# Optimization experiments

Measured on AMD Instinct MI355X. Metric: run time of the kernel, lower is better.

## Reference

```python
import jax, jax.numpy as jnp
import numpy as np

N, E, H, NH = 50000, 800000, 128, 4
D = H // NH
EPS = 1e-5


def _ln(x, g, b):
    m = jnp.mean(x, axis=-1, keepdims=True)
    v = jnp.mean((x - m) ** 2, axis=-1, keepdims=True)
    return (x - m) * jax.lax.rsqrt(v + EPS) * g + b


def setup_inputs() -> dict:
    key = jax.random.key(0)
    ks = jax.random.split(key, 16)

    def lin(k, fi, fo):
        w = jax.random.normal(k, (fi, fo), jnp.float32) * (1.0 / np.sqrt(fi))
        return w, jnp.zeros((fo,), jnp.float32)

    h = jax.random.normal(ks[0], (N, H), jnp.float32)
    e = jax.random.normal(ks[1], (E, H), jnp.float32)
    src = jax.random.randint(ks[2], (E,), 0, N, jnp.int32)
    dst = jax.random.randint(ks[3], (E,), 0, N, jnp.int32)

    Wq, bq = lin(ks[4], H, H)
    Wk, bk = lin(ks[5], 2 * H, H)
    Wv, bv = lin(ks[6], 2 * H, H)
    Wn1, bn1 = lin(ks[7], H, H)
    Wn2, bn2 = lin(ks[8], H, H)
    We1, be1 = lin(ks[9], 3 * H, H)
    We2, be2 = lin(ks[10], H, H)
    gh = jnp.ones((H,), jnp.float32)
    bh = jnp.zeros((H,), jnp.float32)
    ge = jnp.ones((H,), jnp.float32)
    be = jnp.zeros((H,), jnp.float32)

    return dict(h=h, e=e, src=src, dst=dst, Wq=Wq, bq=bq, Wk=Wk, bk=bk,
                Wv=Wv, bv=bv, Wn1=Wn1, bn1=bn1, Wn2=Wn2, bn2=bn2,
                We1=We1, be1=be1, We2=We2, be2=be2, gh=gh, bh=bh, ge=ge, be=be)


def reference(h, e, src, dst, Wq, bq, Wk, bk, Wv, bv, Wn1, bn1, Wn2, bn2,
              We1, be1, We2, be2, gh, bh, ge, be):
    # gather src node features onto edges, concat with edge features: [E, 2H]
    m = jnp.concatenate([h[src], e], axis=-1)
    Q = (h @ Wq + bq).reshape(N, NH, D)
    K = (m @ Wk + bk).reshape(E, NH, D)
    V = (m @ Wv + bv).reshape(E, NH, D)

    # per-edge multihead attention score against destination query: [E, NH]
    s = jnp.sum(Q[dst] * K, axis=-1) / np.sqrt(D).astype(np.float32)

    # destination-grouped (segment) softmax per head
    smax = jax.ops.segment_max(s, dst, num_segments=N)  # [N, NH]
    a = jnp.exp(s - smax[dst])
    denom = jax.ops.segment_sum(a, dst, num_segments=N)  # [N, NH]
    a = a / denom[dst]

    # weighted scatter-sum of values back to destination nodes
    msg = V * a[..., None]  # [E, NH, D]
    h_agg = jax.ops.segment_sum(msg, dst, num_segments=N).reshape(N, H)

    # node MLP update (dropout = identity in eval) + residual + LayerNorm
    h_new = jax.nn.relu(jax.nn.relu(h_agg @ Wn1 + bn1) @ Wn2 + bn2)
    h_out = _ln(h + h_new, gh, bh)

    # edge MLP update on [src_h, dst_h, e] + residual + LayerNorm
    me = jnp.concatenate([h_out[src], h_out[dst], e], axis=-1)  # [E, 3H]
    e_new = jax.nn.relu(jax.nn.relu(me @ We1 + be1) @ We2 + be2)
    e_out = _ln(e + e_new, ge, be)
    return h_out, e_out
```

## Files before the change

### kernel.cpp

```cpp
#include <hip/hip_runtime.h>
#include <hip/hip_bf16.h>

#define NN 50000
#define EE 800000
#define HH 128

typedef __attribute__((ext_vector_type(8))) short bf16x8;
typedef __attribute__((ext_vector_type(4))) float f32x4;

__device__ inline unsigned short f2bf(float f) {
    union { float f; unsigned u; } v; v.f = f;
    unsigned r = v.u + 0x7FFF + ((v.u >> 16) & 1);
    return (unsigned short)(r >> 16);
}

__global__ __launch_bounds__(256) void hist_k(const int* __restrict__ dst, int* __restrict__ cnt) {
    int i = blockIdx.x * 256 + threadIdx.x;
    if (i < EE) atomicAdd(&cnt[dst[i]], 1);
}

__global__ __launch_bounds__(256) void blocksum_k(const int* __restrict__ cnt, int* __restrict__ bsum) {
    __shared__ int sm[256];
    int i = blockIdx.x * 256 + threadIdx.x;
    sm[threadIdx.x] = (i < NN) ? cnt[i] : 0;
    __syncthreads();
    for (int s = 128; s > 0; s >>= 1) {
        if (threadIdx.x < s) sm[threadIdx.x] += sm[threadIdx.x + s];
        __syncthreads();
    }
    if (threadIdx.x == 0) bsum[blockIdx.x] = sm[0];
}

__global__ __launch_bounds__(256) void scanb_k(int* __restrict__ bsum, int nb) {
    __shared__ int sm[256];
    int t = threadIdx.x;
    sm[t] = (t < nb) ? bsum[t] : 0;
    __syncthreads();
    for (int d = 1; d < 256; d <<= 1) {
        int v = (t >= d) ? sm[t - d] : 0;
        __syncthreads();
        sm[t] += v;
        __syncthreads();
    }
    if (t < nb) bsum[t] = sm[t];
}

__global__ __launch_bounds__(256) void offsets_k(const int* __restrict__ cnt, const int* __restrict__ bsum,
                                                 int* __restrict__ offsets, int* __restrict__ cursor) {
    __shared__ int sm[256];
    int b = blockIdx.x, t = threadIdx.x;
    int i = b * 256 + t;
    int c = (i < NN) ? cnt[i] : 0;
    sm[t] = c;
    __syncthreads();
    for (int d = 1; d < 256; d <<= 1) {
        int v = (t >= d) ? sm[t - d] : 0;
        __syncthreads();
        sm[t] += v;
        __syncthreads();
    }
    int incl = sm[t];
    int base = (b == 0) ? 0 : bsum[b - 1];
    int off = base + incl - c;
    if (i < NN) { offsets[i] = off; cursor[i] = off; }
    if (i == NN - 1) offsets[NN] = off + c;
}

__global__ __launch_bounds__(256) void fill_k(const int* __restrict__ src, const int* __restrict__ dst,
                                              int* __restrict__ cursor, int* __restrict__ eids,
                                              int* __restrict__ srcc, int* __restrict__ dstc) {
    int i = blockIdx.x * 256 + threadIdx.x;
    if (i < EE) {
        int d = dst[i];
        int p = atomicAdd(&cursor[d], 1);
        eids[p] = i;
        srcc[p] = src[i];
        dstc[p] = d;
    }
}

__global__ __launch_bounds__(256) void wprep_k(const float* __restrict__ W, unsigned short* __restrict__ out,
                                               int fi, int fo, int n_off, int out_ld) {
    int i = blockIdx.x * 256 + threadIdx.x;
    if (i >= fi * fo) return;
    int n = i / fi, k = i - n * fi;
    out[(size_t)(n_off + n) * out_ld + k] = f2bf(W[(size_t)k * fo + n]);
}

__global__ __launch_bounds__(256) void cvt_k(const float* __restrict__ in, unsigned short* __restrict__ out,
                                             long n8) {
    long i = (long)blockIdx.x * 256 + threadIdx.x;
    if (i >= n8) return;
    const float4* p = (const float4*)in + i * 2;
    float4 a = p[0], b = p[1];
    bf16x8 o = {(short)f2bf(a.x), (short)f2bf(a.y), (short)f2bf(a.z), (short)f2bf(a.w),
                (short)f2bf(b.x), (short)f2bf(b.y), (short)f2bf(b.z), (short)f2bf(b.w)};
    *((bf16x8*)out + i) = o;
}

template <int G, int NCW, int RT, int MODE>
__global__ __launch_bounds__(512, 2) void mm4_k(
    const unsigned short* __restrict__ A0, const int* __restrict__ idx0,
    const unsigned short* __restrict__ Wt, const float* __restrict__ bias,
    int M,
    float* __restrict__ Cf, unsigned short* __restrict__ Cb, int out_ld)
{
    constexpr int RW = 8 / NCW;
    constexpr int ROWS = RW * RT * 16;
    constexpr int Ktot = G * 128;
    constexpr int SI = ROWS / 32;
    __shared__ unsigned short Asl[G * ROWS * 128];

    const int t = threadIdx.x;
    const int wid = t >> 6, lane = t & 63;
    const int lr = lane & 15, lk = lane >> 4;
    const int colw = wid & 3;
    const int roww = wid >> 2;
    const int col0 = colw << 5;
    const int tbase = blockIdx.x * ROWS;

    #pragma unroll
    for (int g = 0; g < G; ++g) {
        #pragma unroll
        for (int i = 0; i < SI; ++i) {
            int rl = ((i * 8 + wid) << 2) + (lane >> 4);
            int gr = tbase + rl; if (gr >= M) gr = M - 1;
            int rid = idx0 ? idx0[gr] : gr;
            const unsigned short* src = A0 + (size_t)rid * HH + (((lane & 15) ^ (rl & 7)) << 3);
            unsigned short* dst = &Asl[(g * ROWS + ((i * 8 + wid) << 2)) << 7];
            __builtin_amdgcn_global_load_lds((const __attribute__((address_space(1))) void*)src,
                                             (__attribute__((address_space(3))) void*)dst, 16, 0, 0);
        }
    }

    f32x4 acc[RT][2];
    #pragma unroll
    for (int tt = 0; tt < RT; ++tt) { acc[tt][0] = (f32x4){0,0,0,0}; acc[tt][1] = (f32x4){0,0,0,0}; }

    __syncthreads();

    #pragma unroll
    for (int g = 0; g < G; ++g) {
        bf16x8 b[4][2];
        #pragma unroll
        for (int s = 0; s < 4; ++s)
            #pragma unroll
            for (int c = 0; c < 2; ++c)
                b[s][c] = *(const bf16x8*)(Wt + (size_t)(col0 + (c << 4) + lr) * Ktot + (g << 7) + (s << 5) + (lk << 3));

        #pragma unroll
        for (int tt = 0; tt < RT; ++tt) {
            const int tl = (tt * RW + roww) << 4;
            bf16x8 a[4];
            #pragma unroll
            for (int s = 0; s < 4; ++s) {
                const int c16 = ((s << 2) + lk) ^ (lr & 7);
                a[s] = *(const bf16x8*)&Asl[((g * ROWS + tl + lr) << 7) + (c16 << 3)];
            }
            #pragma unroll
            for (int s = 0; s < 4; ++s) {
                acc[tt][0] = __builtin_amdgcn_mfma_f32_16x16x32_bf16(a[s], b[s][0], acc[tt][0], 0, 0, 0);
                acc[tt][1] = __builtin_amdgcn_mfma_f32_16x16x32_bf16(a[s], b[s][1], acc[tt][1], 0, 0, 0);
            }
        }
    }

    float bias2[2] = {bias[col0 + lr], bias[col0 + 16 + lr]};
    #pragma unroll
    for (int tt = 0; tt < RT; ++tt) {
        #pragma unroll
        for (int rr = 0; rr < 4; ++rr) {
            int row = tbase + ((tt * RW + roww) << 4) + (lk << 2) + rr;
            if (row >= M) continue;
            #pragma unroll
            for (int c = 0; c < 2; ++c) {
                float v = acc[tt][c][rr] + bias2[c];
                if (MODE == 1) v = fmaxf(v, 0.f);
                size_t o = (size_t)row * out_ld + col0 + (c << 4) + lr;
                if (MODE == 0 || MODE == 1) Cf[o] = v;
                else Cb[o] = f2bf(v);
            }
        }
    }
}

template <int G, int RT>
__global__ __launch_bounds__(512, 2) void mlp_k(
    const unsigned short* __restrict__ A0, const int* __restrict__ idx0,
    const unsigned short* __restrict__ A1, const int* __restrict__ idx1,
    const unsigned short* __restrict__ A2, const int* __restrict__ idx2,
    const unsigned short* __restrict__ W1t, const float* __restrict__ b1,
    const unsigned short* __restrict__ W2t, const float* __restrict__ b2,
    int M,
    float* __restrict__ Cf, unsigned short* __restrict__ Cb2,
    const float* __restrict__ resid, const float* __restrict__ gamma, const float* __restrict__ beta)
{
    constexpr int RW = 2, NCW = 4;
    constexpr int ROWS = RW * RT * 16;
    constexpr int K1 = G * 128;
    constexpr int SI = ROWS / 32;
    __shared__ unsigned short Asl[G * ROWS * 128];
    __shared__ float lnbuf[RT * 32 * 8];

    const int t = threadIdx.x;
    const int wid = t >> 6, lane = t & 63;
    const int lr = lane & 15, lk = lane >> 4;
    const int colw = wid & 3, roww = wid >> 2;
    const int col0 = colw << 5;
    const int tbase = blockIdx.x * ROWS;

    const unsigned short* As[3] = {A0, A1, A2};
    const int* igs[3] = {idx0, idx1, idx2};

    #pragma unroll
    for (int g = 0; g < G; ++g) {
        const unsigned short* Ag = As[g];
        const int* ig = igs[g];
        #pragma unroll
        for (int i = 0; i < SI; ++i) {
            int rl = ((i * 8 + wid) << 2) + (lane >> 4);
            int gr = tbase + rl; if (gr >= M) gr = M - 1;
            int rid = ig ? ig[gr] : gr;
            const unsigned short* src = Ag + (size_t)rid * HH + (((lane & 15) ^ (rl & 7)) << 3);
            unsigned short* dst = &Asl[(g * ROWS + ((i * 8 + wid) << 2)) << 7];
            __builtin_amdgcn_global_load_lds((const __attribute__((address_space(1))) void*)src,
                                             (__attribute__((address_space(3))) void*)dst, 16, 0, 0);
        }
    }

    f32x4 acc[RT][2];
    #pragma unroll
    for (int tt = 0; tt < RT; ++tt) { acc[tt][0] = (f32x4){0,0,0,0}; acc[tt][1] = (f32x4){0,0,0,0}; }

    __syncthreads();

    #pragma unroll
    for (int g = 0; g < G; ++g) {
        bf16x8 b[4][2];
        #pragma unroll
        for (int s = 0; s < 4; ++s)
            #pragma unroll
            for (int c = 0; c < 2; ++c)
                b[s][c] = *(const bf16x8*)(W1t + (size_t)(col0 + (c << 4) + lr) * K1 + (g << 7) + (s << 5) + (lk << 3));

        #pragma unroll
        for (int tt = 0; tt < RT; ++tt) {
            const int tl = (tt * RW + roww) << 4;
            bf16x8 a[4];
            #pragma unroll
            for (int s = 0; s < 4; ++s) {
                const int c16 = ((s << 2) + lk) ^ (lr & 7);
                a[s] = *(const bf16x8*)&Asl[((g * ROWS + tl + lr) << 7) + (c16 << 3)];
            }
            #pragma unroll
            for (int s = 0; s < 4; ++s) {
                acc[tt][0] = __builtin_amdgcn_mfma_f32_16x16x32_bf16(a[s], b[s][0], acc[tt][0], 0, 0, 0);
                acc[tt][1] = __builtin_amdgcn_mfma_f32_16x16x32_bf16(a[s], b[s][1], acc[tt][1], 0, 0, 0);
            }
        }
    }

    __syncthreads();

    {
        float b1c[2] = {b1[col0 + lr], b1[col0 + 16 + lr]};
        #pragma unroll
        for (int tt = 0; tt < RT; ++tt) {
            #pragma unroll
            for (int rr = 0; rr < 4; ++rr) {
                int rowl = ((tt * RW + roww) << 4) + (lk << 2) + rr;
                #pragma unroll
                for (int c = 0; c < 2; ++c) {
                    int col = col0 + (c << 4) + lr;
                    int chunk = (col >> 3) ^ (rowl & 7);
                    Asl[(rowl << 7) + (chunk << 3) + (col & 7)] =
                        f2bf(fmaxf(acc[tt][c][rr] + b1c[c], 0.f));
                }
            }
        }
    }

    __syncthreads();

    f32x4 acc2[RT][2];
    #pragma unroll
    for (int tt = 0; tt < RT; ++tt) { acc2[tt][0] = (f32x4){0,0,0,0}; acc2[tt][1] = (f32x4){0,0,0,0}; }

    {
        bf16x8 b[4][2];
        #pragma unroll
        for (int s = 0; s < 4; ++s)
            #pragma unroll
            for (int c = 0; c < 2; ++c)
                b[s][c] = *(const bf16x8*)(W2t + (size_t)(col0 + (c << 4) + lr) * 128 + (s << 5) + (lk << 3));

        #pragma unroll
        for (int tt = 0; tt < RT; ++tt) {
            const int tl = (tt * RW + roww) << 4;
            bf16x8 a[4];
            #pragma unroll
            for (int s = 0; s < 4; ++s) {
                const int c16 = ((s << 2) + lk) ^ (lr & 7);
                a[s] = *(const bf16x8*)&Asl[((tl + lr) << 7) + (c16 << 3)];
            }
            #pragma unroll
            for (int s = 0; s < 4; ++s) {
                acc2[tt][0] = __builtin_amdgcn_mfma_f32_16x16x32_bf16(a[s], b[s][0], acc2[tt][0], 0, 0, 0);
                acc2[tt][1] = __builtin_amdgcn_mfma_f32_16x16x32_bf16(a[s], b[s][1], acc2[tt][1], 0, 0, 0);
            }
        }
    }

    float b2c[2] = {b2[col0 + lr], b2[col0 + 16 + lr]};
    float g2[2] = {gamma[col0 + lr], gamma[col0 + 16 + lr]};
    float be2[2] = {beta[col0 + lr], beta[col0 + 16 + lr]};

    #pragma unroll
    for (int tt = 0; tt < RT; ++tt) {
        #pragma unroll
        for (int rr = 0; rr < 4; ++rr) {
            int row = tbase + ((tt * RW + roww) << 4) + (lk << 2) + rr;
            int rowc = (row < M) ? row : M - 1;
            float sum = 0.f, sq = 0.f;
            #pragma unroll
            for (int c = 0; c < 2; ++c) {
                float v = fmaxf(acc2[tt][c][rr] + b2c[c], 0.f);
                v += resid[(size_t)rowc * HH + col0 + (c << 4) + lr];
                acc2[tt][c][rr] = v;
                sum += v; sq += v * v;
            }
            sum += __shfl_xor(sum, 1); sq += __shfl_xor(sq, 1);
            sum += __shfl_xor(sum, 2); sq += __shfl_xor(sq, 2);
            sum += __shfl_xor(sum, 4); sq += __shfl_xor(sq, 4);
            sum += __shfl_xor(sum, 8); sq += __shfl_xor(sq, 8);
            if (lr == 0) {
                int rls = (roww << 4) + (lk << 2) + rr;
                lnbuf[((tt * 32 + rls) << 3) + (colw << 1) + 0] = sum;
                lnbuf[((tt * 32 + rls) << 3) + (colw << 1) + 1] = sq;
            }
        }
    }
    __syncthreads();
    #pragma unroll
    for (int tt = 0; tt < RT; ++tt) {
        #pragma unroll
        for (int rr = 0; rr < 4; ++rr) {
            int rls = (roww << 4) + (lk << 2) + rr;
            float s4 = 0.f, q4 = 0.f;
            #pragma unroll
            for (int cw = 0; cw < 4; ++cw) {
                s4 += lnbuf[((tt * 32 + rls) << 3) + (cw << 1) + 0];
                q4 += lnbuf[((tt * 32 + rls) << 3) + (cw << 1) + 1];
            }
            const float mean = s4 * (1.f / 128.f);
            const float var = q4 * (1.f / 128.f) - mean * mean;
            const float rs = rsqrtf(var + 1e-5f);
            int row = tbase + ((tt * RW + roww) << 4) + (lk << 2) + rr;
            if (row < M) {
                #pragma unroll
                for (int c = 0; c < 2; ++c) {
                    float o = (acc2[tt][c][rr] - mean) * rs * g2[c] + be2[c];
                    size_t idx = (size_t)row * HH + col0 + (c << 4) + lr;
                    Cf[idx] = o;
                    if (Cb2) Cb2[idx] = f2bf(o);
                }
            }
        }
    }
}

template <int RT>
__global__ __launch_bounds__(512, 2) void kv_k(
    const unsigned short* __restrict__ hbf, const int* __restrict__ srcc,
    const int* __restrict__ eids, const unsigned short* __restrict__ ebf,
    const unsigned short* __restrict__ Wt, const float* __restrict__ bias,
    const float* __restrict__ Q, const int* __restrict__ dstc,
    int M, unsigned short* __restrict__ V, float* __restrict__ sbuf)
{
    constexpr int ROWS = RT * 16;
    constexpr int Ktot = 256;
    constexpr int SI = ROWS / 32;
    __shared__ unsigned short Asl[2 * ROWS * 128];

    const int t = threadIdx.x;
    const int wid = t >> 6, lane = t & 63;
    const int lr = lane & 15, lk = lane >> 4;
    const int col0 = wid << 5;
    const int tbase = blockIdx.x * ROWS;

    int dstid[RT][4];
    if (wid < 4) {
        #pragma unroll
        for (int tt = 0; tt < RT; ++tt)
            #pragma unroll
            for (int rr = 0; rr < 4; ++rr) {
                int row = tbase + (tt << 4) + (lk << 2) + rr;
                dstid[tt][rr] = dstc[(row < M) ? row : M - 1];
            }
    }

    #pragma unroll
    for (int g = 0; g < 2; ++g) {
        const unsigned short* Ag = g ? ebf : hbf;
        const int* ig = g ? eids : srcc;
        #pragma unroll
        for (int i = 0; i < SI; ++i) {
            int rl = ((i * 8 + wid) << 2) + (lane >> 4);
            int gr = tbase + rl; if (gr >= M) gr = M - 1;
            int rid = ig[gr];
            const unsigned short* srcp = Ag + (size_t)rid * HH + (((lane & 15) ^ (rl & 7)) << 3);
            unsigned short* dstp = &Asl[(g * ROWS + ((i * 8 + wid) << 2)) << 7];
            __builtin_amdgcn_global_load_lds((const __attribute__((address_space(1))) void*)srcp,
                                             (__attribute__((address_space(3))) void*)dstp, 16, 0, 0);
        }
    }

    f32x4 acc[RT][2];
    #pragma unroll
    for (int tt = 0; tt < RT; ++tt) { acc[tt][0] = (f32x4){0,0,0,0}; acc[tt][1] = (f32x4){0,0,0,0}; }

    __syncthreads();

    #pragma unroll
    for (int g = 0; g < 2; ++g) {
        bf16x8 b[4][2];
        #pragma unroll
        for (int s = 0; s < 4; ++s)
            #pragma unroll
            for (int c = 0; c < 2; ++c)
                b[s][c] = *(const bf16x8*)(Wt + (size_t)(col0 + (c << 4) + lr) * Ktot + (g << 7) + (s << 5) + (lk << 3));

        #pragma unroll
        for (int tt = 0; tt < RT; ++tt) {
            bf16x8 a[4];
            #pragma unroll
            for (int s = 0; s < 4; ++s) {
                const int c16 = ((s << 2) + lk) ^ (lr & 7);
                a[s] = *(const bf16x8*)&Asl[((g * ROWS + (tt << 4) + lr) << 7) + (c16 << 3)];
            }
            #pragma unroll
            for (int s = 0; s < 4; ++s) {
                acc[tt][0] = __builtin_amdgcn_mfma_f32_16x16x32_bf16(a[s], b[s][0], acc[tt][0], 0, 0, 0);
                acc[tt][1] = __builtin_amdgcn_mfma_f32_16x16x32_bf16(a[s], b[s][1], acc[tt][1], 0, 0, 0);
            }
        }
    }

    float bias2[2] = {bias[col0 + lr], bias[col0 + 16 + lr]};

    if (wid < 4) {
        #pragma unroll
        for (int tt = 0; tt < RT; ++tt) {
            #pragma unroll
            for (int rr = 0; rr < 4; ++rr) {
                int row = tbase + (tt << 4) + (lk << 2) + rr;
                int d = dstid[tt][rr];
                float q0 = Q[(size_t)d * HH + col0 + lr];
                float q1 = Q[(size_t)d * HH + col0 + 16 + lr];
                float p = (acc[tt][0][rr] + bias2[0]) * q0 + (acc[tt][1][rr] + bias2[1]) * q1;
                p += __shfl_xor(p, 1); p += __shfl_xor(p, 2);
                p += __shfl_xor(p, 4); p += __shfl_xor(p, 8);
                if (lr == 0 && row < M)
                    sbuf[(size_t)row * 4 + wid] = p * 0.17677669529663687f;
            }
        }
    } else {
        #pragma unroll
        for (int tt = 0; tt < RT; ++tt) {
            #pragma unroll
            for (int rr = 0; rr < 4; ++rr) {
                int row = tbase + (tt << 4) + (lk << 2) + rr;
                if (row >= M) continue;
                #pragma unroll
                for (int c = 0; c < 2; ++c)
                    V[(size_t)row * HH + (col0 - 128) + (c << 4) + lr] = f2bf(acc[tt][c][rr] + bias2[c]);
            }
        }
    }
}

__global__ __launch_bounds__(256) void agg_k(const __hip_bfloat16* __restrict__ Vb,
                                             const float* __restrict__ s,
                                             const int* __restrict__ offsets,
                                             unsigned short* __restrict__ hagg)
{
    const int t = threadIdx.x;
    const int n = blockIdx.x * 4 + (t >> 6);
    if (n >= NN) return;
    const int lane = t & 63;
    const int c0 = lane, c1 = lane + 64;
    const int h0 = lane >> 5, h1 = h0 + 2;
    const int o0 = offsets[n], o1 = offsets[n + 1];
    float m0 = -1e30f, m1 = -1e30f, d0 = 0.f, d1 = 0.f, a0 = 0.f, a1 = 0.f;
    for (int j = o0; j < o1; ++j) {
        const float s0 = s[(size_t)j * 4 + h0];
        const float s1 = s[(size_t)j * 4 + h1];
        const float v0 = __bfloat162float(Vb[(size_t)j * HH + c0]);
        const float v1 = __bfloat162float(Vb[(size_t)j * HH + c1]);
        float nm = fmaxf(m0, s0);
        float sc = __expf(m0 - nm);
        float w  = __expf(s0 - nm);
        d0 = d0 * sc + w; a0 = a0 * sc + w * v0; m0 = nm;
        nm = fmaxf(m1, s1);
        sc = __expf(m1 - nm);
        w  = __expf(s1 - nm);
        d1 = d1 * sc + w; a1 = a1 * sc + w * v1; m1 = nm;
    }
    const bool any = (o1 > o0);
    hagg[(size_t)n * HH + c0] = any ? f2bf(a0 / d0) : 0;
    hagg[(size_t)n * HH + c1] = any ? f2bf(a1 / d1) : 0;
}

extern "C" void kernel_launch(void* const* d_in, const int* in_sizes, int n_in,
                              void* d_out, int out_size, void* d_ws, size_t ws_size,
                              hipStream_t stream)
{
    const float* h   = (const float*)d_in[0];
    const float* e   = (const float*)d_in[1];
    const int*   src = (const int*)d_in[2];
    const int*   dst = (const int*)d_in[3];
    const float* Wq  = (const float*)d_in[4];
    const float* bq  = (const float*)d_in[5];
    const float* Wk  = (const float*)d_in[6];
    const float* bk  = (const float*)d_in[7];
    const float* Wv  = (const float*)d_in[8];
    const float* bv  = (const float*)d_in[9];
    const float* Wn1 = (const float*)d_in[10];
    const float* bn1 = (const float*)d_in[11];
    const float* Wn2 = (const float*)d_in[12];
    const float* bn2 = (const float*)d_in[13];
    const float* We1 = (const float*)d_in[14];
    const float* be1 = (const float*)d_in[15];
    const float* We2 = (const float*)d_in[16];
    const float* be2 = (const float*)d_in[17];
    const float* gh  = (const float*)d_in[18];
    const float* bh  = (const float*)d_in[19];
    const float* ge  = (const float*)d_in[20];
    const float* be_ = (const float*)d_in[21];
    (void)in_sizes; (void)n_in; (void)out_size; (void)ws_size;

    float* h_out = (float*)d_out;
    float* e_out = (float*)d_out + (size_t)NN * HH;

    char* ws = (char*)d_ws;
    size_t off = 0;
    auto carve = [&](size_t bytes) { void* p = ws + off; off += (bytes + 255) & ~(size_t)255; return p; };
    unsigned short* Vbuf = (unsigned short*)carve((size_t)EE * HH * 2);
    unsigned short* ebf = (unsigned short*)carve((size_t)EE * HH * 2);
    float* Q      = (float*)carve((size_t)NN * HH * 4);
    float* sbuf   = (float*)carve((size_t)EE * 4 * 4);
    unsigned short* hagg = (unsigned short*)carve((size_t)NN * HH * 2);
    unsigned short* hobf = (unsigned short*)carve((size_t)NN * HH * 2);
    unsigned short* hbf  = (unsigned short*)carve((size_t)NN * HH * 2);
    int* cursor   = (int*)carve((size_t)NN * 4);
    int* offsets  = (int*)carve((size_t)(NN + 1) * 4);
    int* bsum     = (int*)carve(256 * 4);
    int* eids     = (int*)carve((size_t)EE * 4);
    int* srcc     = (int*)carve((size_t)EE * 4);
    int* dstc     = (int*)carve((size_t)EE * 4);
    unsigned short* Wq_s  = (unsigned short*)carve(128 * 128 * 2);
    unsigned short* Wkv_s = (unsigned short*)carve(256 * 256 * 2);
    unsigned short* Wn1_s = (unsigned short*)carve(128 * 128 * 2);
    unsigned short* Wn2_s = (unsigned short*)carve(128 * 128 * 2);
    unsigned short* We1_s = (unsigned short*)carve(128 * 384 * 2);
    unsigned short* We2_s = (unsigned short*)carve(128 * 128 * 2);
    float* b_kv   = (float*)carve(256 * 4);

    const int nb = (NN + 255) / 256;

    wprep_k<<<(128 * 128 + 255) / 256, 256, 0, stream>>>(Wq,  Wq_s,  128, 128, 0, 128);
    wprep_k<<<(256 * 128 + 255) / 256, 256, 0, stream>>>(Wk,  Wkv_s, 256, 128, 0, 256);
    wprep_k<<<(256 * 128 + 255) / 256, 256, 0, stream>>>(Wv,  Wkv_s, 256, 128, 128, 256);
    wprep_k<<<(128 * 128 + 255) / 256, 256, 0, stream>>>(Wn1, Wn1_s, 128, 128, 0, 128);
    wprep_k<<<(128 * 128 + 255) / 256, 256, 0, stream>>>(Wn2, Wn2_s, 128, 128, 0, 128);
    wprep_k<<<(384 * 128 + 255) / 256, 256, 0, stream>>>(We1, We1_s, 384, 128, 0, 384);
    wprep_k<<<(128 * 128 + 255) / 256, 256, 0, stream>>>(We2, We2_s, 128, 128, 0, 128);
    hipMemcpyAsync(b_kv,       bk, 128 * 4, hipMemcpyDeviceToDevice, stream);
    hipMemcpyAsync(b_kv + 128, bv, 128 * 4, hipMemcpyDeviceToDevice, stream);

    cvt_k<<<(NN * HH / 8 + 255) / 256, 256, 0, stream>>>(h, hbf, (long)NN * HH / 8);
    cvt_k<<<(EE * HH / 8 + 255) / 256, 256, 0, stream>>>(e, ebf, (long)EE * HH / 8);

    hipMemsetAsync(cursor, 0, (size_t)NN * 4, stream);
    hist_k<<<(EE + 255) / 256, 256, 0, stream>>>(dst, cursor);
    blocksum_k<<<nb, 256, 0, stream>>>(cursor, bsum);
    scanb_k<<<1, 256, 0, stream>>>(bsum, nb);
    offsets_k<<<nb, 256, 0, stream>>>(cursor, bsum, offsets, cursor);
    fill_k<<<(EE + 255) / 256, 256, 0, stream>>>(src, dst, cursor, eids, srcc, dstc);

    mm4_k<1, 4, 4, 0><<<(NN + 127) / 128, 512, 0, stream>>>(
        hbf, nullptr, Wq_s, bq, NN, Q, nullptr, 128);

    kv_k<4><<<EE / 64, 512, 0, stream>>>(
        hbf, srcc, eids, ebf, Wkv_s, b_kv, Q, dstc, EE, Vbuf, sbuf);

    agg_k<<<(NN + 3) / 4, 256, 0, stream>>>((const __hip_bfloat16*)Vbuf, sbuf, offsets, hagg);

    mlp_k<1, 4><<<(NN + 127) / 128, 512, 0, stream>>>(
        hagg, nullptr, nullptr, nullptr, nullptr, nullptr,
        Wn1_s, bn1, Wn2_s, bn2, NN, h_out, hobf, h, gh, bh);

    mlp_k<3, 2><<<EE / 64, 512, 0, stream>>>(
        hobf, src, hobf, dst, ebf, nullptr,
        We1_s, be1, We2_s, be2, EE, e_out, nullptr, e, ge, be_);
}
```

Measured before the change: 1.278 ms.

## Convert edges to bf16 in CSR order and fuse fp32 edge load into edge MLP

A new conversion kernel writes bf16 edge features already permuted into destination-sorted order. The K/V kernel can then read them contiguously instead of gathering through eids. The edge MLP becomes a dedicated kernel that stages fp32 e into LDS once, converts it to bf16 in registers for the third GEMM K-block, and reuses the same LDS copy for the residual. This removes the full-array bf16 conversion and the separate fp32 residual reread. It costs about 32KB more LDS per block and adds per-use float-to-bf16 conversion work inside the MLP.

```diff
diff --git a/kernel.cpp b/kernel.cpp
--- a/kernel.cpp
+++ b/kernel.cpp
@@ -96,6 +96,20 @@
     bf16x8 o = {(short)f2bf(a.x), (short)f2bf(a.y), (short)f2bf(a.z), (short)f2bf(a.w),
                 (short)f2bf(b.x), (short)f2bf(b.y), (short)f2bf(b.z), (short)f2bf(b.w)};
     *((bf16x8*)out + i) = o;
+}
+
+__global__ __launch_bounds__(256) void cvtcsr_k(const float* __restrict__ e, const int* __restrict__ eids,
+                                                unsigned short* __restrict__ out) {
+    long gid = (long)blockIdx.x * 256 + threadIdx.x;
+    long j = gid >> 4;
+    if (j >= EE) return;
+    int part = (int)(gid & 15);
+    int rid = eids[j];
+    const float4* p = (const float4*)(e + (size_t)rid * HH + part * 8);
+    float4 a = p[0], b = p[1];
+    bf16x8 o = {(short)f2bf(a.x), (short)f2bf(a.y), (short)f2bf(a.z), (short)f2bf(a.w),
+                (short)f2bf(b.x), (short)f2bf(b.y), (short)f2bf(b.z), (short)f2bf(b.w)};
+    *((bf16x8*)(out + (size_t)j * HH + part * 8)) = o;
 }
 
 template <int G, int NCW, int RT, int MODE>
@@ -187,8 +201,6 @@
 template <int G, int RT>
 __global__ __launch_bounds__(512, 2) void mlp_k(
     const unsigned short* __restrict__ A0, const int* __restrict__ idx0,
-    const unsigned short* __restrict__ A1, const int* __restrict__ idx1,
-    const unsigned short* __restrict__ A2, const int* __restrict__ idx2,
     const unsigned short* __restrict__ W1t, const float* __restrict__ b1,
     const unsigned short* __restrict__ W2t, const float* __restrict__ b2,
     int M,
@@ -209,19 +221,14 @@
     const int col0 = colw << 5;
     const int tbase = blockIdx.x * ROWS;
 
-    const unsigned short* As[3] = {A0, A1, A2};
-    const int* igs[3] = {idx0, idx1, idx2};
-
     #pragma unroll
     for (int g = 0; g < G; ++g) {
-        const unsigned short* Ag = As[g];
-        const int* ig = igs[g];
         #pragma unroll
         for (int i = 0; i < SI; ++i) {
             int rl = ((i * 8 + wid) << 2) + (lane >> 4);
             int gr = tbase + rl; if (gr >= M) gr = M - 1;
-            int rid = ig ? ig[gr] : gr;
-            const unsigned short* src = Ag + (size_t)rid * HH + (((lane & 15) ^ (rl & 7)) << 3);
+            int rid = idx0 ? idx0[gr] : gr;
+            const unsigned short* src = A0 + (size_t)rid * HH + (((lane & 15) ^ (rl & 7)) << 3);
             unsigned short* dst = &Asl[(g * ROWS + ((i * 8 + wid) << 2)) << 7];
             __builtin_amdgcn_global_load_lds((const __attribute__((address_space(1))) void*)src,
                                              (__attribute__((address_space(3))) void*)dst, 16, 0, 0);
@@ -369,10 +376,217 @@
     }
 }
 
+__global__ __launch_bounds__(512, 2) void mlpe_k(
+    const unsigned short* __restrict__ ho, const int* __restrict__ src,
+    const int* __restrict__ dst, const float* __restrict__ e,
+    const unsigned short* __restrict__ W1t, const float* __restrict__ b1,
+    const unsigned short* __restrict__ W2t, const float* __restrict__ b2,
+    int M,
+    float* __restrict__ Cf,
+    const float* __restrict__ gamma, const float* __restrict__ beta)
+{
+    constexpr int RW = 2, RT = 2;
+    constexpr int ROWS = RW * RT * 16;
+    constexpr int K1 = 384;
+    __shared__ unsigned short Asl[2 * ROWS * 128];
+    __shared__ float Esl[ROWS * 128];
+    __shared__ float lnbuf[RT * 32 * 8];
+
+    const int t = threadIdx.x;
+    const int wid = t >> 6, lane = t & 63;
+    const int lr = lane & 15, lk = lane >> 4;
+    const int colw = wid & 3, roww = wid >> 2;
+    const int col0 = colw << 5;
+    const int tbase = blockIdx.x * ROWS;
+
+    #pragma unroll
+    for (int g = 0; g < 2; ++g) {
+        const int* ig = g ? dst : src;
+        #pragma unroll
+        for (int i = 0; i < 2; ++i) {
+            int rl = ((i * 8 + wid) << 2) + (lane >> 4);
+            int gr = tbase + rl; if (gr >= M) gr = M - 1;
+            int rid = ig[gr];
+            const unsigned short* sp = ho + (size_t)rid * HH + (((lane & 15) ^ (rl & 7)) << 3);
+            unsigned short* dp = &Asl[(g * ROWS + ((i * 8 + wid) << 2)) << 7];
+            __builtin_amdgcn_global_load_lds((const __attribute__((address_space(1))) void*)sp,
+                                             (__attribute__((address_space(3))) void*)dp, 16, 0, 0);
+        }
+    }
+    #pragma unroll
+    for (int i = 0; i < 4; ++i) {
+        int row = i * 16 + wid * 2 + (lane >> 5);
+        int c16 = lane & 31;
+        int c16s = (c16 & 24) | ((c16 & 7) ^ (row & 7));
+        int gr = tbase + row; if (gr >= M) gr = M - 1;
+        const float* sp = e + (size_t)gr * HH + c16s * 4;
+        float* dp = &Esl[(i * 16 + wid * 2) * 128 + (lane >> 5) * 128];
+        dp = &Esl[(i * 512 + wid * 64) * 4 / 4] + 0;
+        float* dbase = Esl + (size_t)(i * 512 + wid * 64) * 4;
+        (void)dp;
+        __builtin_amdgcn_global_load_lds((const __attribute__((address_space(1))) void*)sp,
+                                         (__attribute__((address_space(3))) void*)dbase, 16, 0, 0);
+    }
+
+    f32x4 acc[RT][2];
+    #pragma unroll
+    for (int tt = 0; tt < RT; ++tt) { acc[tt][0] = (f32x4){0,0,0,0}; acc[tt][1] = (f32x4){0,0,0,0}; }
+
+    __syncthreads();
+
+    #pragma unroll
+    for (int g = 0; g < 3; ++g) {
+        bf16x8 b[4][2];
+        #pragma unroll
+        for (int s = 0; s < 4; ++s)
+            #pragma unroll
+            for (int c = 0; c < 2; ++c)
+                b[s][c] = *(const bf16x8*)(W1t + (size_t)(col0 + (c << 4) + lr) * K1 + (g << 7) + (s << 5) + (lk << 3));
+
+        #pragma unroll
+        for (int tt = 0; tt < RT; ++tt) {
+            const int tl = (tt * RW + roww) << 4;
+            const int r = tl + lr;
+            bf16x8 a[4];
+            if (g < 2) {
+                #pragma unroll
+                for (int s = 0; s < 4; ++s) {
+                    const int c16 = ((s << 2) + lk) ^ (lr & 7);
+                    a[s] = *(const bf16x8*)&Asl[((g * ROWS + r) << 7) + (c16 << 3)];
+                }
+            } else {
+                #pragma unroll
+                for (int s = 0; s < 4; ++s) {
+                    int c16a = (s << 3) + (lk << 1);
+                    int c16b = c16a + 1;
+                    int ca = (c16a & 24) | ((c16a & 7) ^ (r & 7));
+                    int cb = (c16b & 24) | ((c16b & 7) ^ (r & 7));
+                    float4 fa = *(const float4*)&Esl[r * 128 + ca * 4];
+                    float4 fb = *(const float4*)&Esl[r * 128 + cb * 4];
+                    a[s] = (bf16x8){(short)f2bf(fa.x), (short)f2bf(fa.y), (short)f2bf(fa.z), (short)f2bf(fa.w),
+                                    (short)f2bf(fb.x), (short)f2bf(fb.y), (short)f2bf(fb.z), (short)f2bf(fb.w)};
+                }
+            }
+            #pragma unroll
+            for (int s = 0; s < 4; ++s) {
+                acc[tt][0] = __builtin_amdgcn_mfma_f32_16x16x32_bf16(a[s], b[s][0], acc[tt][0], 0, 0, 0);
+                acc[tt][1] = __builtin_amdgcn_mfma_f32_16x16x32_bf16(a[s], b[s][1], acc[tt][1], 0, 0, 0);
+            }
+        }
+    }
+
+    __syncthreads();
+
+    {
+        float b1c[2] = {b1[col0 + lr], b1[col0 + 16 + lr]};
+        #pragma unroll
+        for (int tt = 0; tt < RT; ++tt) {
+            #pragma unroll
+            for (int rr = 0; rr < 4; ++rr) {
+                int rowl = ((tt * RW + roww) << 4) + (lk << 2) + rr;
+                #pragma unroll
+                for (int c = 0; c < 2; ++c) {
+                    int col = col0 + (c << 4) + lr;
+                    int chunk = (col >> 3) ^ (rowl & 7);
+                    Asl[(rowl << 7) + (chunk << 3) + (col & 7)] =
+                        f2bf(fmaxf(acc[tt][c][rr] + b1c[c], 0.f));
+                }
+            }
+        }
+    }
+
+    __syncthreads();
+
+    f32x4 acc2[RT][2];
+    #pragma unroll
+    for (int tt = 0; tt < RT; ++tt) { acc2[tt][0] = (f32x4){0,0,0,0}; acc2[tt][1] = (f32x4){0,0,0,0}; }
+
+    {
+        bf16x8 b[4][2];
+        #pragma unroll
+        for (int s = 0; s < 4; ++s)
+            #pragma unroll
+            for (int c = 0; c < 2; ++c)
+                b[s][c] = *(const bf16x8*)(W2t + (size_t)(col0 + (c << 4) + lr) * 128 + (s << 5) + (lk << 3));
+
+        #pragma unroll
+        for (int tt = 0; tt < RT; ++tt) {
+            const int tl = (tt * RW + roww) << 4;
+            bf16x8 a[4];
+            #pragma unroll
+            for (int s = 0; s < 4; ++s) {
+                const int c16 = ((s << 2) + lk) ^ (lr & 7);
+                a[s] = *(const bf16x8*)&Asl[((tl + lr) << 7) + (c16 << 3)];
+            }
+            #pragma unroll
+            for (int s = 0; s < 4; ++s) {
+                acc2[tt][0] = __builtin_amdgcn_mfma_f32_16x16x32_bf16(a[s], b[s][0], acc2[tt][0], 0, 0, 0);
+                acc2[tt][1] = __builtin_amdgcn_mfma_f32_16x16x32_bf16(a[s], b[s][1], acc2[tt][1], 0, 0, 0);
+            }
+        }
+    }
+
+    float b2c[2] = {b2[col0 + lr], b2[col0 + 16 + lr]};
+    float g2[2] = {gamma[col0 + lr], gamma[col0 + 16 + lr]};
+    float be2[2] = {beta[col0 + lr], beta[col0 + 16 + lr]};
+
+    #pragma unroll
+    for (int tt = 0; tt < RT; ++tt) {
+        #pragma unroll
+        for (int rr = 0; rr < 4; ++rr) {
+            int rowl = ((tt * RW + roww) << 4) + (lk << 2) + rr;
+            float sum = 0.f, sq = 0.f;
+            #pragma unroll
+            for (int c = 0; c < 2; ++c) {
+                int col = col0 + (c << 4) + lr;
+                int c16 = col >> 2;
+                int cs = (c16 & 24) | ((c16 & 7) ^ (rowl & 7));
+                float rv = Esl[rowl * 128 + cs * 4 + (col & 3)];
+                float v = fmaxf(acc2[tt][c][rr] + b2c[c], 0.f) + rv;
+                acc2[tt][c][rr] = v;
+                sum += v; sq += v * v;
+            }
+            sum += __shfl_xor(sum, 1); sq += __shfl_xor(sq, 1);
+            sum += __shfl_xor(sum, 2); sq += __shfl_xor(sq, 2);
+            sum += __shfl_xor(sum, 4); sq += __shfl_xor(sq, 4);
+            sum += __shfl_xor(sum, 8); sq += __shfl_xor(sq, 8);
+            if (lr == 0) {
+                int rls = (roww << 4) + (lk << 2) + rr;
+                lnbuf[((tt * 32 + rls) << 3) + (colw << 1) + 0] = sum;
+                lnbuf[((tt * 32 + rls) << 3) + (colw << 1) + 1] = sq;
+            }
+        }
+    }
+    __syncthreads();
+    #pragma unroll
+    for (int tt = 0; tt < RT; ++tt) {
+        #pragma unroll
+        for (int rr = 0; rr < 4; ++rr) {
+            int rls = (roww << 4) + (lk << 2) + rr;
+            float s4 = 0.f, q4 = 0.f;
+            #pragma unroll
+            for (int cw = 0; cw < 4; ++cw) {
+                s4 += lnbuf[((tt * 32 + rls) << 3) + (cw << 1) + 0];
+                q4 += lnbuf[((tt * 32 + rls) << 3) + (cw << 1) + 1];
+            }
+            const float mean = s4 * (1.f / 128.f);
+            const float var = q4 * (1.f / 128.f) - mean * mean;
+            const float rs = rsqrtf(var + 1e-5f);
+            int row = tbase + ((tt * RW + roww) << 4) + (lk << 2) + rr;
+            if (row < M) {
+                #pragma unroll
+                for (int c = 0; c < 2; ++c)
+                    Cf[(size_t)row * HH + col0 + (c << 4) + lr] =
+                        (acc2[tt][c][rr] - mean) * rs * g2[c] + be2[c];
+            }
+        }
+    }
+}
+
 template <int RT>
 __global__ __launch_bounds__(512, 2) void kv_k(
     const unsigned short* __restrict__ hbf, const int* __restrict__ srcc,
-    const int* __restrict__ eids, const unsigned short* __restrict__ ebf,
+    const unsigned short* __restrict__ ebfc,
     const unsigned short* __restrict__ Wt, const float* __restrict__ bias,
     const float* __restrict__ Q, const int* __restrict__ dstc,
     int M, unsigned short* __restrict__ V, float* __restrict__ sbuf)
@@ -401,13 +615,12 @@
 
     #pragma unroll
     for (int g = 0; g < 2; ++g) {
-        const unsigned short* Ag = g ? ebf : hbf;
-        const int* ig = g ? eids : srcc;
+        const unsigned short* Ag = g ? ebfc : hbf;
         #pragma unroll
         for (int i = 0; i < SI; ++i) {
             int rl = ((i * 8 + wid) << 2) + (lane >> 4);
             int gr = tbase + rl; if (gr >= M) gr = M - 1;
-            int rid = ig[gr];
+            int rid = g ? gr : srcc[gr];
             const unsigned short* srcp = Ag + (size_t)rid * HH + (((lane & 15) ^ (rl & 7)) << 3);
             unsigned short* dstp = &Asl[(g * ROWS + ((i * 8 + wid) << 2)) << 7];
             __builtin_amdgcn_global_load_lds((const __attribute__((address_space(1))) void*)srcp,
@@ -546,7 +759,7 @@
     size_t off = 0;
     auto carve = [&](size_t bytes) { void* p = ws + off; off += (bytes + 255) & ~(size_t)255; return p; };
     unsigned short* Vbuf = (unsigned short*)carve((size_t)EE * HH * 2);
-    unsigned short* ebf = (unsigned short*)carve((size_t)EE * HH * 2);
+    unsigned short* ebfc = (unsigned short*)carve((size_t)EE * HH * 2);
     float* Q      = (float*)carve((size_t)NN * HH * 4);
     float* sbuf   = (float*)carve((size_t)EE * 4 * 4);
     unsigned short* hagg = (unsigned short*)carve((size_t)NN * HH * 2);
@@ -579,7 +792,6 @@
     hipMemcpyAsync(b_kv + 128, bv, 128 * 4, hipMemcpyDeviceToDevice, stream);
 
     cvt_k<<<(NN * HH / 8 + 255) / 256, 256, 0, stream>>>(h, hbf, (long)NN * HH / 8);
-    cvt_k<<<(EE * HH / 8 + 255) / 256, 256, 0, stream>>>(e, ebf, (long)EE * HH / 8);
 
     hipMemsetAsync(cursor, 0, (size_t)NN * 4, stream);
     hist_k<<<(EE + 255) / 256, 256, 0, stream>>>(dst, cursor);
@@ -588,19 +800,19 @@
     offsets_k<<<nb, 256, 0, stream>>>(cursor, bsum, offsets, cursor);
     fill_k<<<(EE + 255) / 256, 256, 0, stream>>>(src, dst, cursor, eids, srcc, dstc);
 
+    cvtcsr_k<<<(EE * 16 + 255) / 256, 256, 0, stream>>>(e, eids, ebfc);
+
     mm4_k<1, 4, 4, 0><<<(NN + 127) / 128, 512, 0, stream>>>(
         hbf, nullptr, Wq_s, bq, NN, Q, nullptr, 128);
 
     kv_k<4><<<EE / 64, 512, 0, stream>>>(
-        hbf, srcc, eids, ebf, Wkv_s, b_kv, Q, dstc, EE, Vbuf, sbuf);
+        hbf, srcc, ebfc, Wkv_s, b_kv, Q, dstc, EE, Vbuf, sbuf);
 
     agg_k<<<(NN + 3) / 4, 256, 0, stream>>>((const __hip_bfloat16*)Vbuf, sbuf, offsets, hagg);
 
     mlp_k<1, 4><<<(NN + 127) / 128, 512, 0, stream>>>(
-        hagg, nullptr, nullptr, nullptr, nullptr, nullptr,
-        Wn1_s, bn1, Wn2_s, bn2, NN, h_out, hobf, h, gh, bh);
-
-    mlp_k<3, 2><<<EE / 64, 512, 0, stream>>>(
-        hobf, src, hobf, dst, ebf, nullptr,
-        We1_s, be1, We2_s, be2, EE, e_out, nullptr, e, ge, be_);
-}
+        hagg, nullptr, Wn1_s, bn1, Wn2_s, bn2, NN, h_out, hobf, h, gh, bh);
+
+    mlpe_k<<<EE / 64, 512, 0, stream>>>(
+        hobf, src, dst, e, We1_s, be1, We2_s, be2, EE, e_out, ge, be_);
+}
```

Measured after the change: 1.246 ms. 1.03x faster.
